# Performance work log

Measured on AMD Instinct MI355X. Metric: run time of the kernel, lower is better.

## Reference

```python
import jax, jax.numpy as jnp
import numpy as np

EPS = 1e-6


def _mlp(x, Ws, bs):
    # 5-layer MLP, exact (erf) GELU between layers, matching torch.nn.GELU()
    for W, b in zip(Ws[:-1], bs[:-1]):
        x = jax.nn.gelu(x @ W + b, approximate=False)
    return x @ Ws[-1] + bs[-1]


def setup_inputs() -> dict:
    key = jax.random.key(0)
    ks = jax.random.split(key, 16)
    B, H, D, NT = 262144, 256, 128, 16
    # deformation gradient near identity -> det(F) > 0 so log(det) is finite
    F = jnp.eye(3, dtype=jnp.float32)[None] + 0.05 * jax.random.normal(ks[0], (B, 3, 3), dtype=jnp.float32)
    C = 0.1 * jax.random.normal(ks[1], (B, 3, 3), dtype=jnp.float32)
    emb = 0.02 * jax.random.normal(ks[2], (NT, D), dtype=jnp.float32)
    dims = [16 + 9 + D, H, H, H, H, 9]
    inp = {"F": F, "C": C, "emb": emb, "traj_ids": 3}
    for i in range(5):
        inp[f"W{i+1}"] = jax.random.normal(ks[3 + 2 * i], (dims[i], dims[i + 1]), dtype=jnp.float32) / np.sqrt(dims[i]).astype(np.float32)
        inp[f"b{i+1}"] = jnp.zeros((dims[i + 1],), dtype=jnp.float32)
    return inp


def reference(F, C, emb, traj_ids, W1, b1, W2, b2, W3, b3, W4, b4, W5, b5):
    B = F.shape[0]
    U, sigma, Vh = jnp.linalg.svd(F)          # batched 3x3 SVD
    R = U @ Vh                                 # polar rotation, == torch U @ V^T
    Ft = jnp.swapaxes(F, -1, -2)
    FtF = Ft @ F
    det = jnp.linalg.det(F)
    f00 = jnp.maximum(F[:, 0, 0], EPS)
    # normalize_input=True branch: subtract 1 from each invariant
    I1 = sigma - 1.0                                   # [B,3]
    I2 = (FtF - jnp.eye(3, dtype=F.dtype)).reshape(B, 9)
    I3 = det[:, None] - 1.0
    I4 = jnp.log(det)[:, None] - 1.0
    I5 = f00[:, None] - 1.0
    I6 = jnp.log(f00)[:, None] - 1.0
    strain = jnp.concatenate([I1, I2, I3, I4, I5, I6], axis=1)  # [B,16]
    latent = jnp.broadcast_to(emb[traj_ids][None, :], (B, emb.shape[1]))
    feats = jnp.concatenate([strain, C.reshape(B, 9), latent], axis=-1)
    out = _mlp(feats, [W1, W2, W3, W4, W5], [b1, b2, b3, b4, b5])  # [B,9]
    x = out.reshape(B, 3, 3)
    x = 0.5 * (jnp.swapaxes(x, -1, -2) + x)    # symmetrize
    P = R @ x
    cauchy = P @ Ft
    return cauchy
```

## Files before the change

kernel.cpp:

```cpp
#include <hip/hip_runtime.h>

typedef _Float16 f16;
typedef _Float16 f16x8 __attribute__((ext_vector_type(8)));
typedef float f32x4 __attribute__((ext_vector_type(4)));
typedef float f32x16 __attribute__((ext_vector_type(16)));

#define MROWS 64
#define THREADS 512
#define HSTR 264

#define WS_B1EFF 0
#define WS_W1H   1024
#define WS_W2H   (WS_W1H + 16384)
#define WS_W3H   (WS_W2H + 131072)
#define WS_W4H   (WS_W3H + 131072)
#define WS_W5H   (WS_W4H + 131072)
#define WS_END   (WS_W5H + 8192)

__global__ void prep_kernel(const float* __restrict__ emb, const int* __restrict__ traj,
                            const float* __restrict__ W1, const float* __restrict__ b1,
                            const float* __restrict__ W2, const float* __restrict__ W3,
                            const float* __restrict__ W4, const float* __restrict__ W5,
                            float* __restrict__ b1eff,
                            f16* __restrict__ W1h, f16* __restrict__ W2h,
                            f16* __restrict__ W3h, f16* __restrict__ W4h,
                            f16* __restrict__ W5h) {
  if (blockIdx.x == 816) {
    __shared__ float lat[128];
    int t = *traj;
    if (threadIdx.x < 128) lat[threadIdx.x] = emb[t * 128 + threadIdx.x];
    __syncthreads();
    int n = threadIdx.x;
    float s0 = 0.f, s1 = 0.f, s2 = 0.f, s3 = 0.f;
#pragma unroll 4
    for (int d = 0; d < 128; d += 4) {
      s0 = fmaf(lat[d + 0], W1[(25 + d) * 256 + n], s0);
      s1 = fmaf(lat[d + 1], W1[(26 + d) * 256 + n], s1);
      s2 = fmaf(lat[d + 2], W1[(27 + d) * 256 + n], s2);
      s3 = fmaf(lat[d + 3], W1[(28 + d) * 256 + n], s3);
    }
    b1eff[n] = b1[n] + ((s0 + s1) + (s2 + s3));
    return;
  }
  int i = blockIdx.x * 256 + threadIdx.x;
  if (i < 8192) {
    int n = i >> 5, k = i & 31;
    W1h[i] = (f16)((k < 25) ? W1[k * 256 + n] : 0.0f);
  } else if (i < 73728) {
    int j = i - 8192; int k = j >> 8, n = j & 255;
    W2h[n * 256 + k] = (f16)W2[j];
  } else if (i < 139264) {
    int j = i - 73728; int k = j >> 8, n = j & 255;
    W3h[n * 256 + k] = (f16)W3[j];
  } else if (i < 204800) {
    int j = i - 139264; int k = j >> 8, n = j & 255;
    W4h[n * 256 + k] = (f16)W4[j];
  } else if (i < 208896) {
    int j = i - 204800; int n = j >> 8, k = j & 255;
    W5h[j] = (f16)((n < 9) ? W5[k * 9 + n] : 0.0f);
  }
}

__device__ __forceinline__ float gelu_exact(float z) {
  float s = z * z;
  float q = fmaf(s, -1.8889263e-5f, 2.30872094e-4f);
  q = fmaf(s, q, -0.0023746714834f);
  q = fmaf(s, q, 0.01994711402007f);
  q = fmaf(s, q, -0.13298076013381f);
  q = fmaf(s, q, 0.79788456080287f);
  float t = z * q;
  float u = 0.5f * z;
  return fmaf(u, t, u);
}

__global__ __launch_bounds__(THREADS, 6) void fused_kernel(
    const float* __restrict__ Fg, const float* __restrict__ Cg,
    const f16* __restrict__ W1h, const f16* __restrict__ W2h,
    const f16* __restrict__ W3h, const f16* __restrict__ W4h,
    const f16* __restrict__ W5h,
    const float* __restrict__ b1eff, const float* __restrict__ b2,
    const float* __restrict__ b3, const float* __restrict__ b4,
    const float* __restrict__ b5, float* __restrict__ outg, int Btot) {
  __shared__ __align__(16) char sFeat[4096];
  __shared__ __align__(16) f16 hA[64 * HSTR];
  __shared__ __align__(16) float o32[64 * 16];
  __shared__ __align__(16) float sR[64 * 9];

  const int tid = threadIdx.x;
  const int lane = tid & 63;
  const int wv = tid >> 6;
  const int quad = lane >> 4;
  const int l15 = lane & 15;
  const int l31 = lane & 31;
  const int kh = lane >> 5;
  const int row0 = blockIdx.x * MROWS;

  if (tid < MROWS) {
    const int grow = row0 + tid;
    float feat[25];
    float Rm[9];
    if (grow < Btot) {
      float Fm[9], Cm[9];
      const float* fp = Fg + grow * 9;
      const float* cp = Cg + grow * 9;
#pragma unroll
      for (int i = 0; i < 9; ++i) Fm[i] = fp[i];
#pragma unroll
      for (int i = 0; i < 9; ++i) Cm[i] = cp[i];
      float G[9];
#pragma unroll
      for (int i = 0; i < 3; ++i)
#pragma unroll
        for (int j = 0; j < 3; ++j)
          G[i * 3 + j] = Fm[i] * Fm[j] + Fm[3 + i] * Fm[3 + j] + Fm[6 + i] * Fm[6 + j];
      float det = Fm[0] * (Fm[4] * Fm[8] - Fm[5] * Fm[7])
                - Fm[1] * (Fm[3] * Fm[8] - Fm[5] * Fm[6])
                + Fm[2] * (Fm[3] * Fm[7] - Fm[4] * Fm[6]);
#pragma unroll
      for (int i = 0; i < 9; ++i) Rm[i] = Fm[i];
#pragma unroll
      for (int it = 0; it < 5; ++it) {
        float c0 = Rm[4]*Rm[8] - Rm[5]*Rm[7];
        float c1 = Rm[5]*Rm[6] - Rm[3]*Rm[8];
        float c2 = Rm[3]*Rm[7] - Rm[4]*Rm[6];
        float c3 = Rm[2]*Rm[7] - Rm[1]*Rm[8];
        float c4 = Rm[0]*Rm[8] - Rm[2]*Rm[6];
        float c5 = Rm[1]*Rm[6] - Rm[0]*Rm[7];
        float c6 = Rm[1]*Rm[5] - Rm[2]*Rm[4];
        float c7 = Rm[2]*Rm[3] - Rm[0]*Rm[5];
        float c8 = Rm[0]*Rm[4] - Rm[1]*Rm[3];
        float dr = Rm[0]*c0 + Rm[1]*c1 + Rm[2]*c2;
        float hv = 0.5f / dr;
        Rm[0] = 0.5f*Rm[0] + hv*c0; Rm[1] = 0.5f*Rm[1] + hv*c1; Rm[2] = 0.5f*Rm[2] + hv*c2;
        Rm[3] = 0.5f*Rm[3] + hv*c3; Rm[4] = 0.5f*Rm[4] + hv*c4; Rm[5] = 0.5f*Rm[5] + hv*c5;
        Rm[6] = 0.5f*Rm[6] + hv*c6; Rm[7] = 0.5f*Rm[7] + hv*c7; Rm[8] = 0.5f*Rm[8] + hv*c8;
      }
      float s00 = Rm[0]*Fm[0] + Rm[3]*Fm[3] + Rm[6]*Fm[6];
      float s11 = Rm[1]*Fm[1] + Rm[4]*Fm[4] + Rm[7]*Fm[7];
      float s22 = Rm[2]*Fm[2] + Rm[5]*Fm[5] + Rm[8]*Fm[8];
      float s01 = 0.5f*((Rm[0]*Fm[1]+Rm[3]*Fm[4]+Rm[6]*Fm[7]) + (Rm[1]*Fm[0]+Rm[4]*Fm[3]+Rm[7]*Fm[6]));
      float s02 = 0.5f*((Rm[0]*Fm[2]+Rm[3]*Fm[5]+Rm[6]*Fm[8]) + (Rm[2]*Fm[0]+Rm[5]*Fm[3]+Rm[8]*Fm[6]));
      float s12 = 0.5f*((Rm[1]*Fm[2]+Rm[4]*Fm[5]+Rm[7]*Fm[8]) + (Rm[2]*Fm[1]+Rm[5]*Fm[4]+Rm[8]*Fm[7]));
      float q  = (s00 + s11 + s22) * (1.0f/3.0f);
      float p1 = s01*s01 + s02*s02 + s12*s12;
      float d0 = s00 - q, d1 = s11 - q, d2 = s22 - q;
      float p2 = d0*d0 + d1*d1 + d2*d2 + 2.0f*p1;
      float p  = sqrtf(p2 * (1.0f/6.0f));
      float e1, e2, e3;
      if (p > 1e-10f) {
        float pi = 1.0f / p;
        float b00 = d0*pi, b11 = d1*pi, b22 = d2*pi;
        float b01 = s01*pi, b02 = s02*pi, b12 = s12*pi;
        float detB = b00*(b11*b22 - b12*b12) - b01*(b01*b22 - b12*b02) + b02*(b01*b12 - b11*b02);
        float r = fminf(fmaxf(0.5f*detB, -1.0f), 1.0f);
        float phi = acosf(r) * (1.0f/3.0f);
        e1 = q + 2.0f * p * cosf(phi);
        e3 = q + 2.0f * p * cosf(phi + 2.0943951023931953f);
        e2 = 3.0f*q - e1 - e3;
      } else { e1 = q; e2 = q; e3 = q; }
      float f00 = fmaxf(Fm[0], 1e-6f);
      feat[0] = e1 - 1.0f; feat[1] = e2 - 1.0f; feat[2] = e3 - 1.0f;
#pragma unroll
      for (int k = 0; k < 9; ++k) feat[3 + k] = G[k];
      feat[3] -= 1.0f; feat[7] -= 1.0f; feat[11] -= 1.0f;
      feat[12] = det - 1.0f;
      feat[13] = logf(det) - 1.0f;
      feat[14] = f00 - 1.0f;
      feat[15] = logf(f00) - 1.0f;
#pragma unroll
      for (int k = 0; k < 9; ++k) feat[16 + k] = Cm[k];
    } else {
#pragma unroll
      for (int k = 0; k < 25; ++k) feat[k] = 0.0f;
#pragma unroll
      for (int k = 0; k < 9; ++k) Rm[k] = 0.0f;
    }
#pragma unroll
    for (int k = 0; k < 9; ++k) sR[tid * 9 + k] = Rm[k];
#pragma unroll
    for (int c = 0; c < 4; ++c) {
      f16x8 v;
#pragma unroll
      for (int j = 0; j < 8; ++j) {
        int k = c * 8 + j;
        v[j] = (f16)((k < 25) ? feat[k] : 0.0f);
      }
      *(f16x8*)(sFeat + tid * 64 + c * 16) = v;
    }
  }
  __syncthreads();

  {
#pragma unroll
    for (int t = 0; t < 2; ++t) {
      const int col = wv * 32 + t * 16 + l15;
      f16x8 bfr = *(const f16x8*)(W1h + col * 32 + quad * 8);
      float bias = b1eff[col];
#pragma unroll
      for (int st = 0; st < 4; ++st) {
        const int arow = st * 16 + l15;
        f16x8 a = *(const f16x8*)(sFeat + arow * 64 + quad * 16);
        f32x4 acc = (f32x4){bias, bias, bias, bias};
        acc = __builtin_amdgcn_mfma_f32_16x16x32_f16(a, bfr, acc, 0, 0, 0);
#pragma unroll
        for (int r = 0; r < 4; ++r) {
          const int orow = st * 16 + quad * 4 + r;
          hA[orow * HSTR + col] = (f16)gelu_exact(acc[r]);
        }
      }
    }
  }
  __syncthreads();

  const f16* Whs[3] = {W2h, W3h, W4h};
  const float* bgs[3] = {b2, b3, b4};
  const int col32 = wv * 32 + l31;
#pragma unroll 1
  for (int L = 0; L < 3; ++L) {
    const f16* Wh = Whs[L];
    const float bias = bgs[L][col32];
    f32x16 acc0, acc1;
#pragma unroll
    for (int r = 0; r < 16; ++r) { acc0[r] = bias; acc1[r] = bias; }
#pragma unroll
    for (int q = 0; q < 4; ++q) {
      f16x8 bq[4];
#pragma unroll
      for (int j = 0; j < 4; ++j)
        bq[j] = *(const f16x8*)(Wh + col32 * 256 + (q * 4 + j) * 16 + kh * 8);
#pragma unroll
      for (int j = 0; j < 4; ++j) {
        f16x8 a0 = *(const f16x8*)(hA + l31 * HSTR + (q * 4 + j) * 16 + kh * 8);
        acc0 = __builtin_amdgcn_mfma_f32_32x32x16_f16(a0, bq[j], acc0, 0, 0, 0);
      }
#pragma unroll
      for (int j = 0; j < 4; ++j) {
        f16x8 a1 = *(const f16x8*)(hA + (32 + l31) * HSTR + (q * 4 + j) * 16 + kh * 8);
        acc1 = __builtin_amdgcn_mfma_f32_32x32x16_f16(a1, bq[j], acc1, 0, 0, 0);
      }
    }
    f16 hv0[16], hv1[16];
#pragma unroll
    for (int r = 0; r < 16; ++r) {
      hv0[r] = (f16)gelu_exact(acc0[r]);
      hv1[r] = (f16)gelu_exact(acc1[r]);
    }
    __syncthreads();
#pragma unroll
    for (int r = 0; r < 16; ++r) {
      const int orow = (r & 3) + 8 * (r >> 2) + 4 * kh;
      hA[orow * HSTR + col32] = hv0[r];
      hA[(32 + orow) * HSTR + col32] = hv1[r];
    }
    __syncthreads();
  }

  if (wv < 4) {
    f16x8 bf5[8];
#pragma unroll
    for (int s = 0; s < 8; ++s)
      bf5[s] = *(const f16x8*)(W5h + l15 * 256 + s * 32 + quad * 8);
    const int arow = wv * 16 + l15;
    float bv = (l15 < 9) ? b5[l15] : 0.0f;
    f32x4 acc = (f32x4){bv, bv, bv, bv};
#pragma unroll
    for (int s = 0; s < 8; ++s) {
      f16x8 a = *(const f16x8*)(hA + arow * HSTR + s * 32 + quad * 8);
      acc = __builtin_amdgcn_mfma_f32_16x16x32_f16(a, bf5[s], acc, 0, 0, 0);
    }
#pragma unroll
    for (int r = 0; r < 4; ++r) {
      const int orow = wv * 16 + quad * 4 + r;
      o32[orow * 16 + l15] = acc[r];
    }
  }
  __syncthreads();

  float* stage = (float*)sFeat;
  if (tid < MROWS && row0 + tid < Btot) {
    const float* x = o32 + tid * 16;
    const float* fp = Fg + (row0 + tid) * 9;
    float Fm[9], Rm[9];
#pragma unroll
    for (int i = 0; i < 9; ++i) Fm[i] = fp[i];
#pragma unroll
    for (int i = 0; i < 9; ++i) Rm[i] = sR[tid * 9 + i];
    float y[9];
    y[0] = x[0]; y[4] = x[4]; y[8] = x[8];
    y[1] = 0.5f * (x[1] + x[3]); y[3] = y[1];
    y[2] = 0.5f * (x[2] + x[6]); y[6] = y[2];
    y[5] = 0.5f * (x[5] + x[7]); y[7] = y[5];
    float P[9];
#pragma unroll
    for (int i = 0; i < 3; ++i)
#pragma unroll
      for (int j = 0; j < 3; ++j)
        P[i*3+j] = Rm[i*3]*y[j] + Rm[i*3+1]*y[3+j] + Rm[i*3+2]*y[6+j];
#pragma unroll
    for (int i = 0; i < 3; ++i)
#pragma unroll
      for (int j = 0; j < 3; ++j)
        stage[tid*9 + i*3 + j] = P[i*3]*Fm[j*3] + P[i*3+1]*Fm[j*3+1] + P[i*3+2]*Fm[j*3+2];
  }
  __syncthreads();
  for (int i = tid; i < MROWS * 9; i += THREADS) {
    int gi = row0 * 9 + i;
    if (gi < Btot * 9) outg[gi] = stage[i];
  }
}

extern "C" void kernel_launch(void* const* d_in, const int* in_sizes, int n_in,
                              void* d_out, int out_size, void* d_ws, size_t ws_size,
                              hipStream_t stream) {
  const float* Fg  = (const float*)d_in[0];
  const float* Cg  = (const float*)d_in[1];
  const float* emb = (const float*)d_in[2];
  const int*   trj = (const int*)d_in[3];
  const float* W1  = (const float*)d_in[4];
  const float* b1  = (const float*)d_in[5];
  const float* W2  = (const float*)d_in[6];
  const float* b2  = (const float*)d_in[7];
  const float* W3  = (const float*)d_in[8];
  const float* b3  = (const float*)d_in[9];
  const float* W4  = (const float*)d_in[10];
  const float* b4  = (const float*)d_in[11];
  const float* W5  = (const float*)d_in[12];
  const float* b5  = (const float*)d_in[13];
  float* outg = (float*)d_out;
  const int Btot = in_sizes[0] / 9;

  char* ws = (char*)d_ws;
  float* b1eff = (float*)(ws + WS_B1EFF);
  f16* W1h = (f16*)(ws + WS_W1H);
  f16* W2h = (f16*)(ws + WS_W2H);
  f16* W3h = (f16*)(ws + WS_W3H);
  f16* W4h = (f16*)(ws + WS_W4H);
  f16* W5h = (f16*)(ws + WS_W5H);

  prep_kernel<<<817, 256, 0, stream>>>(emb, trj, W1, b1, W2, W3, W4, W5,
                                       b1eff, W1h, W2h, W3h, W4h, W5h);
  const int grid = (Btot + MROWS - 1) / MROWS;
  fused_kernel<<<grid, THREADS, 0, stream>>>(Fg, Cg, W1h, W2h, W3h, W4h, W5h,
                                             b1eff, b2, b3, b4, b5, outg, Btot);
}
```

Baseline: 314.0 us.

## Double rows per block to 128 to reuse weight fragments across more MFMAs

```diff
diff --git a/kernel.cpp b/kernel.cpp
--- a/kernel.cpp
+++ b/kernel.cpp
@@ -5,7 +5,7 @@
 typedef float f32x4 __attribute__((ext_vector_type(4)));
 typedef float f32x16 __attribute__((ext_vector_type(16)));
 
-#define MROWS 64
+#define MROWS 128
 #define THREADS 512
 #define HSTR 264
 
@@ -73,7 +73,7 @@
   return fmaf(u, t, u);
 }
 
-__global__ __launch_bounds__(THREADS, 6) void fused_kernel(
+__global__ __launch_bounds__(THREADS, 4) void fused_kernel(
     const float* __restrict__ Fg, const float* __restrict__ Cg,
     const f16* __restrict__ W1h, const f16* __restrict__ W2h,
     const f16* __restrict__ W3h, const f16* __restrict__ W4h,
@@ -81,10 +81,9 @@
     const float* __restrict__ b1eff, const float* __restrict__ b2,
     const float* __restrict__ b3, const float* __restrict__ b4,
     const float* __restrict__ b5, float* __restrict__ outg, int Btot) {
-  __shared__ __align__(16) char sFeat[4096];
-  __shared__ __align__(16) f16 hA[64 * HSTR];
-  __shared__ __align__(16) float o32[64 * 16];
-  __shared__ __align__(16) float sR[64 * 9];
+  __shared__ __align__(16) f16 hA[MROWS * HSTR];
+  __shared__ __align__(16) char uFO[MROWS * 64];
+  __shared__ __align__(16) float sR[MROWS * 9];
 
   const int tid = threadIdx.x;
   const int lane = tid & 63;
@@ -185,7 +184,7 @@
         int k = c * 8 + j;
         v[j] = (f16)((k < 25) ? feat[k] : 0.0f);
       }
-      *(f16x8*)(sFeat + tid * 64 + c * 16) = v;
+      *(f16x8*)(uFO + tid * 64 + c * 16) = v;
     }
   }
   __syncthreads();
@@ -197,9 +196,9 @@
       f16x8 bfr = *(const f16x8*)(W1h + col * 32 + quad * 8);
       float bias = b1eff[col];
 #pragma unroll
-      for (int st = 0; st < 4; ++st) {
+      for (int st = 0; st < 8; ++st) {
         const int arow = st * 16 + l15;
-        f16x8 a = *(const f16x8*)(sFeat + arow * 64 + quad * 16);
+        f16x8 a = *(const f16x8*)(uFO + arow * 64 + quad * 16);
         f32x4 acc = (f32x4){bias, bias, bias, bias};
         acc = __builtin_amdgcn_mfma_f32_16x16x32_f16(a, bfr, acc, 0, 0, 0);
 #pragma unroll
@@ -219,9 +218,9 @@
   for (int L = 0; L < 3; ++L) {
     const f16* Wh = Whs[L];
     const float bias = bgs[L][col32];
-    f32x16 acc0, acc1;
-#pragma unroll
-    for (int r = 0; r < 16; ++r) { acc0[r] = bias; acc1[r] = bias; }
+    f32x16 acc0, acc1, acc2, acc3;
+#pragma unroll
+    for (int r = 0; r < 16; ++r) { acc0[r] = bias; acc1[r] = bias; acc2[r] = bias; acc3[r] = bias; }
 #pragma unroll
     for (int q = 0; q < 4; ++q) {
       f16x8 bq[4];
@@ -230,32 +229,47 @@
         bq[j] = *(const f16x8*)(Wh + col32 * 256 + (q * 4 + j) * 16 + kh * 8);
 #pragma unroll
       for (int j = 0; j < 4; ++j) {
-        f16x8 a0 = *(const f16x8*)(hA + l31 * HSTR + (q * 4 + j) * 16 + kh * 8);
-        acc0 = __builtin_amdgcn_mfma_f32_32x32x16_f16(a0, bq[j], acc0, 0, 0, 0);
+        f16x8 a = *(const f16x8*)(hA + l31 * HSTR + (q * 4 + j) * 16 + kh * 8);
+        acc0 = __builtin_amdgcn_mfma_f32_32x32x16_f16(a, bq[j], acc0, 0, 0, 0);
       }
 #pragma unroll
       for (int j = 0; j < 4; ++j) {
-        f16x8 a1 = *(const f16x8*)(hA + (32 + l31) * HSTR + (q * 4 + j) * 16 + kh * 8);
-        acc1 = __builtin_amdgcn_mfma_f32_32x32x16_f16(a1, bq[j], acc1, 0, 0, 0);
-      }
-    }
-    f16 hv0[16], hv1[16];
+        f16x8 a = *(const f16x8*)(hA + (32 + l31) * HSTR + (q * 4 + j) * 16 + kh * 8);
+        acc1 = __builtin_amdgcn_mfma_f32_32x32x16_f16(a, bq[j], acc1, 0, 0, 0);
+      }
+#pragma unroll
+      for (int j = 0; j < 4; ++j) {
+        f16x8 a = *(const f16x8*)(hA + (64 + l31) * HSTR + (q * 4 + j) * 16 + kh * 8);
+        acc2 = __builtin_amdgcn_mfma_f32_32x32x16_f16(a, bq[j], acc2, 0, 0, 0);
+      }
+#pragma unroll
+      for (int j = 0; j < 4; ++j) {
+        f16x8 a = *(const f16x8*)(hA + (96 + l31) * HSTR + (q * 4 + j) * 16 + kh * 8);
+        acc3 = __builtin_amdgcn_mfma_f32_32x32x16_f16(a, bq[j], acc3, 0, 0, 0);
+      }
+    }
+    f16 hv0[16], hv1[16], hv2[16], hv3[16];
 #pragma unroll
     for (int r = 0; r < 16; ++r) {
       hv0[r] = (f16)gelu_exact(acc0[r]);
       hv1[r] = (f16)gelu_exact(acc1[r]);
+      hv2[r] = (f16)gelu_exact(acc2[r]);
+      hv3[r] = (f16)gelu_exact(acc3[r]);
     }
     __syncthreads();
 #pragma unroll
     for (int r = 0; r < 16; ++r) {
       const int orow = (r & 3) + 8 * (r >> 2) + 4 * kh;
-      hA[orow * HSTR + col32] = hv0[r];
+      hA[orow * HSTR + col32]        = hv0[r];
       hA[(32 + orow) * HSTR + col32] = hv1[r];
+      hA[(64 + orow) * HSTR + col32] = hv2[r];
+      hA[(96 + orow) * HSTR + col32] = hv3[r];
     }
     __syncthreads();
   }
 
-  if (wv < 4) {
+  {
+    float* o32 = (float*)uFO;
     f16x8 bf5[8];
 #pragma unroll
     for (int s = 0; s < 8; ++s)
@@ -276,9 +290,10 @@
   }
   __syncthreads();
 
-  float* stage = (float*)sFeat;
+  float* stage = (float*)hA;
+  const float* o32c = (const float*)uFO;
   if (tid < MROWS && row0 + tid < Btot) {
-    const float* x = o32 + tid * 16;
+    const float* x = o32c + tid * 16;
     const float* fp = Fg + (row0 + tid) * 9;
     float Fm[9], Rm[9];
 #pragma unroll
```

Result: faster. 260.2 us (-17.1%).
